# Kernel tuning notes

Measured on AMD Instinct MI355X. Metric: run time of the kernel, lower is better.

The kernel has to match this reference:

```python
import jax, jax.numpy as jnp
import numpy as np

BLOCK_SIZE = 32
HEADS = 8
DIM_HEAD = 64
ROPE_THETA = 10000.0


def rmsnorm(x, w):
    eps = jnp.finfo(x.dtype).eps
    var = jnp.mean(jnp.square(x), axis=-1, keepdims=True)
    return x * jax.lax.rsqrt(var + eps) * w


def rope_cos_sin(seq_len, dim_head):
    # lucidrains rotary-embedding-torch default: interleaved pairs, theta=10000
    inv_freq = 1.0 / (ROPE_THETA ** (jnp.arange(0, dim_head, 2, dtype=jnp.float32) / dim_head))
    freqs = jnp.arange(seq_len, dtype=jnp.float32)[:, None] * inv_freq[None, :]  # [S, Dh/2]
    return jnp.cos(freqs), jnp.sin(freqs)


def apply_rope(t, cos, sin):
    # t: [B, H, S, Dh], cos/sin: [S, Dh/2]
    t1 = t[..., 0::2]
    t2 = t[..., 1::2]
    out = jnp.stack([t1 * cos - t2 * sin, t1 * sin + t2 * cos], axis=-1)
    return out.reshape(t.shape)


def split_heads(x, h):
    b, n, _ = x.shape
    return x.reshape(b, n, h, -1).transpose(0, 2, 1, 3)  # b h n d


def forward(tokens, attn_norm_w, qkv_w, out_w, mix_w, mix_b,
            ff_norm_w, ff_in_w, ff_in_b, ff_out_w, ff_out_b, final_norm_w):
    B, S, D = tokens.shape
    L = qkv_w.shape[0]
    H, Dh = HEADS, DIM_HEAD
    scale = Dh ** -0.5
    cos, sin = rope_cos_sin(S, Dh)

    # block-causal mask: q_idx // block >= kv_idx // block
    idx = jnp.arange(S)
    allowed = (idx[:, None] // BLOCK_SIZE) >= (idx[None, :] // BLOCK_SIZE)  # [S, S] bool
    neg = -jnp.finfo(tokens.dtype).max

    t = tokens
    first_v = None
    for l in range(L):
        # --- block causal attention ---
        x = rmsnorm(t, attn_norm_w[l])
        qkv = x @ qkv_w[l]  # [B, S, 3*H*Dh]
        q, k, v = jnp.split(qkv, 3, axis=-1)
        q, k, v = split_heads(q, H), split_heads(k, H), split_heads(v, H)  # b h s d
        orig_v = v
        if l > 0:
            mix = jax.nn.sigmoid(x @ mix_w[l] + mix_b[l])  # [B, S, H]
            mix = mix.transpose(0, 2, 1)[..., None]  # [B, H, S, 1]
            v = v + mix * (first_v - v)  # lerp
        q = apply_rope(q, cos, sin)
        k = apply_rope(k, cos, sin)
        sim = jnp.einsum('bhid,bhjd->bhij', q * scale, k)
        sim = jnp.where(allowed, sim, neg)
        attn = jax.nn.softmax(sim, axis=-1)
        o = jnp.einsum('bhij,bhjd->bhid', attn, v)
        o = o.transpose(0, 2, 1, 3).reshape(B, S, H * Dh)
        t = t + o @ out_w[l]
        if first_v is None:
            first_v = orig_v
        # --- SwiGLU feedforward ---
        y = rmsnorm(t, ff_norm_w[l])
        h = y @ ff_in_w[l] + ff_in_b[l]
        a, g = jnp.split(h, 2, axis=-1)
        y = (a * jax.nn.gelu(g, approximate=False)) @ ff_out_w[l] + ff_out_b[l]
        t = t + y

    return rmsnorm(t, final_norm_w)


def setup_inputs():
    key = jax.random.key(0)
    B, S, D, L = 2, 2048, 512, 4
    Di = HEADS * DIM_HEAD  # 512
    Dhid = int(D * 4.0 * 2 / 3)  # 1365
    ks = jax.random.split(key, 8)
    s = 0.02
    return {
        'tokens': jax.random.normal(ks[0], (B, S, D), jnp.float32),
        'attn_norm_w': jnp.ones((L, D), jnp.float32),
        'qkv_w': jax.random.normal(ks[1], (L, D, 3 * Di), jnp.float32) * s,
        'out_w': jax.random.normal(ks[2], (L, Di, D), jnp.float32) * s,
        'mix_w': jax.random.normal(ks[3], (L, D, HEADS), jnp.float32) * s,
        'mix_b': jnp.zeros((L, HEADS), jnp.float32),
        'ff_norm_w': jnp.ones((L, D), jnp.float32),
        'ff_in_w': jax.random.normal(ks[4], (L, D, 2 * Dhid), jnp.float32) * s,
        'ff_in_b': jnp.zeros((L, 2 * Dhid), jnp.float32),
        'ff_out_w': jax.random.normal(ks[5], (L, Dhid, D), jnp.float32) * s,
        'ff_out_b': jnp.zeros((L, D), jnp.float32),
        'final_norm_w': jnp.ones((D,), jnp.float32),
    }


def reference(tokens, attn_norm_w, qkv_w, out_w, mix_w, mix_b,
              ff_norm_w, ff_in_w, ff_in_b, ff_out_w, ff_out_b, final_norm_w):
    return forward(tokens, attn_norm_w, qkv_w, out_w, mix_w, mix_b,
                   ff_norm_w, ff_in_w, ff_in_b, ff_out_w, ff_out_b, final_norm_w)
```

## Files before the change

### kernel.cpp

```cpp
#include <hip/hip_runtime.h>
#include <hip/hip_bf16.h>
#include <math.h>

typedef __bf16 bf16;
typedef bf16 bf16x8 __attribute__((ext_vector_type(8)));
typedef float f32x4 __attribute__((ext_vector_type(4)));

#define LDS16(gp, lp) __builtin_amdgcn_global_load_lds( \
    (const __attribute__((address_space(1))) unsigned int*)(gp), \
    (__attribute__((address_space(3))) unsigned int*)(lp), 16, 0, 0)

__device__ __forceinline__ int cumoff(int qt) {
  if (qt < 8)  return qt;
  if (qt < 16) return 8 + 2 * (qt - 8);
  if (qt < 24) return 24 + 3 * (qt - 16);
  return 48 + 4 * (qt - 24);
}

__global__ void convert_w_kernel(const float* __restrict__ W, bf16* __restrict__ WT,
                                 int K, int N, int Kp, int Np,
                                 size_t wstride, size_t wtstride)
{
  __shared__ float tile[32][33];
  const float* Wl = W + blockIdx.z * wstride;
  bf16* WTl = WT + blockIdx.z * wtstride;
  int k0 = blockIdx.x * 32, n0 = blockIdx.y * 32;
  int tx = threadIdx.x, ty = threadIdx.y;
  for (int i = ty; i < 32; i += 8) {
    int k = k0 + i, n = n0 + tx;
    tile[i][tx] = (k < K && n < N) ? Wl[(size_t)k * N + n] : 0.f;
  }
  __syncthreads();
  for (int i = ty; i < 32; i += 8) {
    int n = n0 + i, k = k0 + tx;
    if (n < Np && k < Kp) WTl[(size_t)n * Kp + k] = (bf16)tile[tx][i];
  }
}

__global__ __launch_bounds__(256)
void rope_kernel(float* __restrict__ tab)
{
  int idx = blockIdx.x * 256 + threadIdx.x;
  int s = idx >> 5, j = idx & 31;
  float invf = (float)exp((double)(2 * j) * -0.14391156847064293);
  float ang = (float)s * invf;
  float sn, cs;
  sincosf(ang, &sn, &cs);
  tab[idx] = cs;
  tab[65536 + idx] = sn;
}

template<bool BF16OUT>
__global__ __launch_bounds__(64)
void rmsnorm_kernel(const float* __restrict__ in, const float* __restrict__ wgt,
                    void* __restrict__ outp)
{
  int row = blockIdx.x, lane = threadIdx.x;
  const float* p = in + (size_t)row * 512;
  float4 v0 = *(const float4*)(p + lane * 4);
  float4 v1 = *(const float4*)(p + 256 + lane * 4);
  float ss = v0.x*v0.x + v0.y*v0.y + v0.z*v0.z + v0.w*v0.w
           + v1.x*v1.x + v1.y*v1.y + v1.z*v1.z + v1.w*v1.w;
  #pragma unroll
  for (int d = 1; d < 64; d <<= 1) ss += __shfl_xor(ss, d);
  float sc = rsqrtf(ss * (1.f / 512.f) + 1.1920929e-7f);
  float a0[4] = {v0.x, v0.y, v0.z, v0.w};
  float a1[4] = {v1.x, v1.y, v1.z, v1.w};
  #pragma unroll
  for (int i = 0; i < 4; ++i) {
    int c0 = lane * 4 + i, c1 = 256 + lane * 4 + i;
    float r0 = a0[i] * sc * wgt[c0];
    float r1 = a1[i] * sc * wgt[c1];
    if (BF16OUT) {
      ((bf16*)outp)[(size_t)row * 512 + c0] = (bf16)r0;
      ((bf16*)outp)[(size_t)row * 512 + c1] = (bf16)r1;
    } else {
      ((float*)outp)[(size_t)row * 512 + c0] = r0;
      ((float*)outp)[(size_t)row * 512 + c1] = r1;
    }
  }
}

__global__ __launch_bounds__(256)
void qkvpost_kernel(const float* __restrict__ qkv, const float* __restrict__ mb,
                    const float* __restrict__ rope, float* __restrict__ firstv,
                    bf16* __restrict__ qb, bf16* __restrict__ kb,
                    bf16* __restrict__ vT, int layer)
{
  int idx = blockIdx.x * 256 + threadIdx.x;
  int j = idx & 31;
  int s = (idx >> 5) & 2047;
  int bh = idx >> 16;
  int b = bh >> 3, h = bh & 7;
  size_t row = (size_t)b * 2048 + s;
  const float* base = qkv + row * 1664 + h * 64 + 2 * j;
  float q1 = base[0],    q2 = base[1];
  float k1 = base[512],  k2 = base[513];
  float v1 = base[1024], v2 = base[1025];
  float cs = rope[s * 32 + j];
  float sn = rope[65536 + s * 32 + j];
  size_t qoff = ((size_t)bh * 2048 + s) * 64 + 2 * j;
  qb[qoff]     = (bf16)((q1 * cs - q2 * sn) * 0.125f);
  qb[qoff + 1] = (bf16)((q1 * sn + q2 * cs) * 0.125f);
  kb[qoff]     = (bf16)(k1 * cs - k2 * sn);
  kb[qoff + 1] = (bf16)(k1 * sn + k2 * cs);
  if (layer == 0) {
    firstv[qoff] = v1; firstv[qoff + 1] = v2;
  } else {
    float logit = qkv[row * 1664 + 1536 + h] + mb[h];
    float mx = 1.f / (1.f + __expf(-logit));
    v1 += mx * (firstv[qoff] - v1);
    v2 += mx * (firstv[qoff + 1] - v2);
  }
  vT[((size_t)bh * 64 + 2 * j) * 2048 + s]     = (bf16)v1;
  vT[((size_t)bh * 64 + 2 * j + 1) * 2048 + s] = (bf16)v2;
}

__global__ __launch_bounds__(256, 3)
void attn_kernel(const bf16* __restrict__ Q, const bf16* __restrict__ Kmat,
                 const bf16* __restrict__ VT, float* __restrict__ Opart,
                 float* __restrict__ mlbuf)
{
  __shared__ __align__(16) bf16 smK[2][8 * 512];
  __shared__ __align__(16) bf16 smV[2][8 * 512];
  __shared__ __align__(16) bf16 smP[4][16 * 72];
  const int bid = blockIdx.x;
  const int bh = bid / 80;
  const int r80 = bid - bh * 80;
  int qt, chunk;
  if (r80 < 8)       { qt = r80; chunk = 0; }
  else if (r80 < 24) { qt = 8 + ((r80 - 8) >> 1);  chunk = (r80 - 8) & 1; }
  else if (r80 < 48) { int t = r80 - 24; qt = 16 + t / 3; chunk = t - (qt - 16) * 3; }
  else               { int t = r80 - 48; qt = 24 + (t >> 2); chunk = t & 3; }
  const int jt0 = chunk * 8;
  const int njt = min(jt0 + 8, qt + 1) - jt0;

  const int tid = threadIdx.x;
  const int w = tid >> 6, lane = tid & 63;
  const int c = lane & 15, quad = lane >> 4;

  const size_t qrow0 = (size_t)bh * 2048 + qt * 64 + w * 16;
  bf16x8 aQ0 = *(const bf16x8*)(Q + (qrow0 + c) * 64 + quad * 8);
  bf16x8 aQ1 = *(const bf16x8*)(Q + (qrow0 + c) * 64 + 32 + quad * 8);

  const bf16* Kg = Kmat + ((size_t)bh * 2048 + w * 16 + c) * 64 + quad * 8;
  const bf16* Vg = VT + ((size_t)bh * 64 + w * 16 + c) * 2048 + quad * 8;

  {
    const bf16* kp = Kg + (size_t)jt0 * 4096;
    const bf16* vp = Vg + jt0 * 64;
    LDS16(kp,      smK[0] + w * 1024);
    LDS16(kp + 32, smK[0] + w * 1024 + 512);
    LDS16(vp,      smV[0] + w * 1024);
    LDS16(vp + 32, smV[0] + w * 1024 + 512);
  }

  f32x4 o[4] = {{0,0,0,0},{0,0,0,0},{0,0,0,0},{0,0,0,0}};
  float mrow[4] = {-3.0e38f, -3.0e38f, -3.0e38f, -3.0e38f};
  float lrow[4] = {0.f, 0.f, 0.f, 0.f};

  for (int j = 0; j < njt; ++j) {
    const int b = j & 1;
    const int jt = jt0 + j;
    __syncthreads();
    if (j + 1 < njt) {
      const bf16* kp = Kg + (size_t)(jt + 1) * 4096;
      const bf16* vp = Vg + (jt + 1) * 64;
      bf16* kd = smK[1 - b] + w * 1024;
      bf16* vd = smV[1 - b] + w * 1024;
      LDS16(kp,      kd);
      LDS16(kp + 32, kd + 512);
      LDS16(vp,      vd);
      LDS16(vp + 32, vd + 512);
    }

    f32x4 s[4];
    #pragma unroll
    for (int nt = 0; nt < 4; ++nt) {
      bf16x8 bK0 = *(const bf16x8*)(smK[b] + (nt * 2) * 512 + lane * 8);
      bf16x8 bK1 = *(const bf16x8*)(smK[b] + (nt * 2 + 1) * 512 + lane * 8);
      f32x4 acc = {0.f, 0.f, 0.f, 0.f};
      acc = __builtin_amdgcn_mfma_f32_16x16x32_bf16(aQ0, bK0, acc, 0, 0, 0);
      acc = __builtin_amdgcn_mfma_f32_16x16x32_bf16(aQ1, bK1, acc, 0, 0, 0);
      s[nt] = acc;
    }
    if (jt == qt && w < 2) {
      #pragma unroll
      for (int r = 0; r < 4; ++r) { s[2][r] = -3.0e38f; s[3][r] = -3.0e38f; }
    }

    #pragma unroll
    for (int r = 0; r < 4; ++r) {
      float smax = fmaxf(fmaxf(s[0][r], s[1][r]), fmaxf(s[2][r], s[3][r]));
      #pragma unroll
      for (int d = 1; d < 16; d <<= 1) smax = fmaxf(smax, __shfl_xor(smax, d));
      float mnew = fmaxf(mrow[r], smax);
      float alpha = __expf(mrow[r] - mnew);
      mrow[r] = mnew;
      float p0 = __expf(s[0][r] - mnew);
      float p1 = __expf(s[1][r] - mnew);
      float p2 = __expf(s[2][r] - mnew);
      float p3 = __expf(s[3][r] - mnew);
      float rsum = (p0 + p1) + (p2 + p3);
      #pragma unroll
      for (int d = 1; d < 16; d <<= 1) rsum += __shfl_xor(rsum, d);
      lrow[r] = lrow[r] * alpha + rsum;
      o[0][r] *= alpha; o[1][r] *= alpha; o[2][r] *= alpha; o[3][r] *= alpha;
      bf16* pp = smP[w] + (quad * 4 + r) * 72 + c;
      pp[0]  = (bf16)p0;
      pp[16] = (bf16)p1;
      pp[32] = (bf16)p2;
      pp[48] = (bf16)p3;
    }
    asm volatile("s_waitcnt lgkmcnt(0)" ::: "memory");

    #pragma unroll
    for (int ks2 = 0; ks2 < 2; ++ks2) {
      bf16x8 aP = *(const bf16x8*)(smP[w] + c * 72 + ks2 * 32 + quad * 8);
      #pragma unroll
      for (int nt = 0; nt < 4; ++nt) {
        bf16x8 bV = *(const bf16x8*)(smV[b] + (nt * 2 + ks2) * 512 + lane * 8);
        o[nt] = __builtin_amdgcn_mfma_f32_16x16x32_bf16(aP, bV, o[nt], 0, 0, 0);
      }
    }
  }

  const int slot = bh * 80 + cumoff(qt) + chunk;
  float* Op = Opart + (size_t)slot * 4096;
  #pragma unroll
  for (int r = 0; r < 4; ++r) {
    int row = w * 16 + quad * 4 + r;
    #pragma unroll
    for (int nt = 0; nt < 4; ++nt)
      Op[row * 64 + nt * 16 + c] = o[nt][r];
    if (c == 0) {
      mlbuf[slot * 128 + row] = mrow[r];
      mlbuf[slot * 128 + 64 + row] = lrow[r];
    }
  }
}

__global__ __launch_bounds__(256)
void attn_combine_kernel(const float* __restrict__ Opart, const float* __restrict__ mlbuf,
                         bf16* __restrict__ Omat)
{
  const int qt = blockIdx.x, bh = blockIdx.y;
  const int nch = (qt >> 3) + 1;
  const int base = bh * 80 + cumoff(qt);
  const int tid = threadIdx.x;
  const int row = tid >> 2, cg = tid & 3;

  float mv[4], lv[4];
  float M = -3.0e38f;
  #pragma unroll
  for (int ch = 0; ch < 4; ++ch) {
    if (ch < nch) {
      mv[ch] = mlbuf[(base + ch) * 128 + row];
      lv[ch] = mlbuf[(base + ch) * 128 + 64 + row];
      M = fmaxf(M, mv[ch]);
    } else { mv[ch] = -3.0e38f; lv[ch] = 0.f; }
  }
  float L = 0.f, wgt[4];
  #pragma unroll
  for (int ch = 0; ch < 4; ++ch) {
    wgt[ch] = __expf(mv[ch] - M);
    L += lv[ch] * wgt[ch];
  }
  float inv = 1.f / L;

  f32x4 acc[4] = {{0,0,0,0},{0,0,0,0},{0,0,0,0},{0,0,0,0}};
  #pragma unroll
  for (int ch = 0; ch < 4; ++ch) {
    if (ch < nch) {
      const f32x4* p = (const f32x4*)(Opart + (size_t)(base + ch) * 4096 + row * 64 + cg * 16);
      #pragma unroll
      for (int i = 0; i < 4; ++i) acc[i] += wgt[ch] * p[i];
    }
  }
  const int b = bh >> 3, h = bh & 7;
  bf16* op = Omat + ((size_t)b * 2048 + qt * 64 + row) * 512 + h * 64 + cg * 16;
  #pragma unroll
  for (int i = 0; i < 4; ++i)
    #pragma unroll
    for (int j = 0; j < 4; ++j)
      op[i * 4 + j] = (bf16)(acc[i][j] * inv);
}

template<int MODE>
__global__ __launch_bounds__(256, 2)
void gemm_kernel(const bf16* __restrict__ A, const bf16* __restrict__ WT,
                 const float* __restrict__ bias, int n_bias,
                 const float* __restrict__ Tin, void* __restrict__ outp,
                 int K, int N)
{
  __shared__ __align__(16) bf16 smA[8 * 512];
  __shared__ __align__(16) bf16 smB[8 * 512];
  const int tid = threadIdx.x;
  const int w = tid >> 6, lane = tid & 63;
  const int c = lane & 15, quad = lane >> 4;
  const int wy = w >> 1, wx = w & 1;
  const int bm = blockIdx.y * 128, bn = blockIdx.x * 128;

  f32x4 acc[4][4] = {};

  const bf16* Ag0 = A  + (size_t)(bm + (w * 2)     * 16 + c) * K + quad * 8;
  const bf16* Ag1 = A  + (size_t)(bm + (w * 2 + 1) * 16 + c) * K + quad * 8;
  const bf16* Bg0 = WT + (size_t)(bn + (w * 2)     * 16 + c) * K + quad * 8;
  const bf16* Bg1 = WT + (size_t)(bn + (w * 2 + 1) * 16 + c) * K + quad * 8;
  bf16* la0 = smA + (w * 2) * 512;
  bf16* la1 = smA + (w * 2 + 1) * 512;
  bf16* lb0 = smB + (w * 2) * 512;
  bf16* lb1 = smB + (w * 2 + 1) * 512;

  const int NK = K >> 5;
  for (int kk = 0; kk < NK; ++kk) {
    const int ko = kk * 32;
    LDS16(Ag0 + ko, la0);
    LDS16(Ag1 + ko, la1);
    LDS16(Bg0 + ko, lb0);
    LDS16(Bg1 + ko, lb1);
    __syncthreads();
    bf16x8 af[4], bfr[4];
    #pragma unroll
    for (int mt = 0; mt < 4; ++mt)
      af[mt] = *(const bf16x8*)(smA + (wy * 4 + mt) * 512 + lane * 8);
    #pragma unroll
    for (int nt = 0; nt < 4; ++nt)
      bfr[nt] = *(const bf16x8*)(smB + (wx * 4 + nt) * 512 + lane * 8);
    #pragma unroll
    for (int mt = 0; mt < 4; ++mt)
      #pragma unroll
      for (int nt = 0; nt < 4; ++nt)
        acc[mt][nt] = __builtin_amdgcn_mfma_f32_16x16x32_bf16(af[mt], bfr[nt], acc[mt][nt], 0, 0, 0);
    __syncthreads();
  }

  const int r0 = bm + wy * 64;
  const int c0 = bn + wx * 64;
  #pragma unroll
  for (int mt = 0; mt < 4; ++mt) {
    #pragma unroll
    for (int nt = 0; nt < 4; ++nt) {
      #pragma unroll
      for (int r = 0; r < 4; ++r) {
        size_t row = (size_t)(r0 + mt * 16 + quad * 4 + r);
        int col = c0 + nt * 16 + c;
        float v = acc[mt][nt][r];
        float bv = (bias != nullptr && col < n_bias) ? bias[col] : 0.f;
        if (MODE == 2) {
          ((float*)outp)[row * N + col] = Tin[row * N + col] + v + bv;
        } else if (MODE == 1) {
          ((float*)outp)[row * N + col] = v;
        } else {
          ((bf16*)outp)[row * N + col] = (bf16)(v + bv);
        }
      }
    }
  }
}

template<int MODE>
__global__ __launch_bounds__(256, 4)
void gemm64_kernel(const bf16* __restrict__ A, const bf16* __restrict__ WT,
                   const float* __restrict__ bias, int n_bias,
                   const float* __restrict__ Tin, void* __restrict__ outp,
                   int K, int N)
{
  __shared__ __align__(16) bf16 smA[4 * 512];
  __shared__ __align__(16) bf16 smB[4 * 512];
  const int tid = threadIdx.x;
  const int w = tid >> 6, lane = tid & 63;
  const int c = lane & 15, quad = lane >> 4;
  const int wy = w >> 1, wx = w & 1;
  const int bm = blockIdx.y * 64, bn = blockIdx.x * 64;

  f32x4 acc[2][2] = {};

  const bf16* Ag = A  + (size_t)(bm + w * 16 + c) * K + quad * 8;
  const bf16* Bg = WT + (size_t)(bn + w * 16 + c) * K + quad * 8;
  bf16* la = smA + w * 512;
  bf16* lb = smB + w * 512;

  const int NK = K >> 5;
  for (int kk = 0; kk < NK; ++kk) {
    const int ko = kk * 32;
    LDS16(Ag + ko, la);
    LDS16(Bg + ko, lb);
    __syncthreads();
    bf16x8 af[2], bfr[2];
    #pragma unroll
    for (int mt = 0; mt < 2; ++mt)
      af[mt] = *(const bf16x8*)(smA + (wy * 2 + mt) * 512 + lane * 8);
    #pragma unroll
    for (int nt = 0; nt < 2; ++nt)
      bfr[nt] = *(const bf16x8*)(smB + (wx * 2 + nt) * 512 + lane * 8);
    #pragma unroll
    for (int mt = 0; mt < 2; ++mt)
      #pragma unroll
      for (int nt = 0; nt < 2; ++nt)
        acc[mt][nt] = __builtin_amdgcn_mfma_f32_16x16x32_bf16(af[mt], bfr[nt], acc[mt][nt], 0, 0, 0);
    __syncthreads();
  }

  const int r0 = bm + wy * 32;
  const int c0 = bn + wx * 32;
  #pragma unroll
  for (int mt = 0; mt < 2; ++mt) {
    #pragma unroll
    for (int nt = 0; nt < 2; ++nt) {
      #pragma unroll
      for (int r = 0; r < 4; ++r) {
        size_t row = (size_t)(r0 + mt * 16 + quad * 4 + r);
        int col = c0 + nt * 16 + c;
        float v = acc[mt][nt][r];
        float bv = (bias != nullptr && col < n_bias) ? bias[col] : 0.f;
        if (MODE == 2) {
          ((float*)outp)[row * N + col] = Tin[row * N + col] + v + bv;
        } else if (MODE == 1) {
          ((float*)outp)[row * N + col] = v;
        } else {
          ((bf16*)outp)[row * N + col] = (bf16)(v + bv);
        }
      }
    }
  }
}

__global__ __launch_bounds__(256)
void act_kernel(const bf16* __restrict__ h, bf16* __restrict__ act)
{
  int col = blockIdx.x * 256 + threadIdx.x;
  int row = blockIdx.y;
  if (col >= 1376) return;
  float v = 0.f;
  if (col < 1365) {
    float a = (float)h[(size_t)row * 2816 + col];
    float g = (float)h[(size_t)row * 2816 + 1365 + col];
    v = a * 0.5f * g * (1.f + erff(g * 0.70710678118654752f));
  }
  act[(size_t)row * 1376 + col] = (bf16)v;
}

extern "C" void kernel_launch(void* const* d_in, const int* in_sizes, int n_in,
                              void* d_out, int out_size, void* d_ws, size_t ws_size,
                              hipStream_t stream)
{
  const float* tokens  = (const float*)d_in[0];
  const float* anw     = (const float*)d_in[1];
  const float* qkvw    = (const float*)d_in[2];
  const float* outw    = (const float*)d_in[3];
  const float* mixw    = (const float*)d_in[4];
  const float* mixbias = (const float*)d_in[5];
  const float* fnw     = (const float*)d_in[6];
  const float* ffiw    = (const float*)d_in[7];
  const float* ffib    = (const float*)d_in[8];
  const float* ffow    = (const float*)d_in[9];
  const float* ffob    = (const float*)d_in[10];
  const float* finw    = (const float*)d_in[11];
  float* outp = (float*)d_out;

  char* ws = (char*)d_ws;
  size_t off = 0;
  auto alloc = [&](size_t bytes) -> char* {
    char* p = ws + off;
    off += (bytes + 255) & ~(size_t)255;
    return p;
  };
  bf16* wtq    = (bf16*)alloc((size_t)4 * 1664 * 512 * 2);
  bf16* wto    = (bf16*)alloc((size_t)4 * 512 * 512 * 2);
  bf16* wtfi   = (bf16*)alloc((size_t)4 * 2816 * 512 * 2);
  bf16* wtfo   = (bf16*)alloc((size_t)4 * 512 * 1376 * 2);
  float* tbuf  = (float*)alloc((size_t)4096 * 512 * 4);
  bf16* xb     = (bf16*)alloc((size_t)4096 * 512 * 2);
  bf16* yb     = (bf16*)alloc((size_t)4096 * 512 * 2);
  float* qkvb  = (float*)alloc((size_t)4096 * 1664 * 4);
  float* fv    = (float*)alloc((size_t)16 * 2048 * 64 * 4);
  bf16* qb     = (bf16*)alloc((size_t)16 * 2048 * 64 * 2);
  bf16* kbuf   = (bf16*)alloc((size_t)16 * 2048 * 64 * 2);
  bf16* vT     = (bf16*)alloc((size_t)16 * 2048 * 64 * 2);
  bf16* ob     = (bf16*)alloc((size_t)4096 * 512 * 2);
  bf16* hb     = (bf16*)alloc((size_t)4096 * 2816 * 2);
  bf16* actb   = (bf16*)alloc((size_t)4096 * 1376 * 2);
  float* rope  = (float*)alloc((size_t)2 * 65536 * 4);
  float* mlbuf = (float*)alloc((size_t)1280 * 128 * 4);
  float* Opart = qkvb;

  dim3 tcv(32, 8);
  convert_w_kernel<<<dim3(16, 48, 4), tcv, 0, stream>>>(
      qkvw, wtq, 512, 1536, 512, 1536, (size_t)512 * 1536, (size_t)1664 * 512);
  convert_w_kernel<<<dim3(16, 4, 4), tcv, 0, stream>>>(
      mixw, wtq + (size_t)1536 * 512, 512, 8, 512, 128, (size_t)512 * 8, (size_t)1664 * 512);
  convert_w_kernel<<<dim3(16, 16, 4), tcv, 0, stream>>>(
      outw, wto, 512, 512, 512, 512, (size_t)512 * 512, (size_t)512 * 512);
  convert_w_kernel<<<dim3(16, 88, 4), tcv, 0, stream>>>(
      ffiw, wtfi, 512, 2730, 512, 2816, (size_t)512 * 2730, (size_t)2816 * 512);
  convert_w_kernel<<<dim3(43, 16, 4), tcv, 0, stream>>>(
      ffow, wtfo, 1365, 512, 1376, 512, (size_t)1365 * 512, (size_t)1376 * 512);
  rope_kernel<<<256, 256, 0, stream>>>(rope);
  hipMemcpyAsync(tbuf, tokens, (size_t)4096 * 512 * 4, hipMemcpyDeviceToDevice, stream);

  for (int l = 0; l < 4; ++l) {
    rmsnorm_kernel<true><<<4096, 64, 0, stream>>>(tbuf, anw + l * 512, xb);
    gemm_kernel<1><<<dim3(13, 32), 256, 0, stream>>>(
        xb, wtq + (size_t)l * 1664 * 512, nullptr, 0, nullptr, qkvb, 512, 1664);
    qkvpost_kernel<<<4096, 256, 0, stream>>>(qkvb, mixbias + l * 8, rope, fv, qb, kbuf, vT, l);
    attn_kernel<<<1280, 256, 0, stream>>>(qb, kbuf, vT, Opart, mlbuf);
    attn_combine_kernel<<<dim3(32, 16), 256, 0, stream>>>(Opart, mlbuf, ob);
    gemm64_kernel<2><<<dim3(8, 64), 256, 0, stream>>>(
        ob, wto + (size_t)l * 512 * 512, nullptr, 0, tbuf, tbuf, 512, 512);
    rmsnorm_kernel<true><<<4096, 64, 0, stream>>>(tbuf, fnw + l * 512, yb);
    gemm_kernel<0><<<dim3(22, 32), 256, 0, stream>>>(
        yb, wtfi + (size_t)l * 2816 * 512, ffib + (size_t)l * 2730, 2730, nullptr, hb, 512, 2816);
    act_kernel<<<dim3(6, 4096), 256, 0, stream>>>(hb, actb);
    gemm64_kernel<2><<<dim3(8, 64), 256, 0, stream>>>(
        actb, wtfo + (size_t)l * 512 * 1376, ffob + (size_t)l * 512, 512, tbuf, tbuf, 1376, 512);
  }
  rmsnorm_kernel<false><<<4096, 64, 0, stream>>>(tbuf, finw, outp);
}
```

Measured before the change: 874.2 us.

## Process 128 query rows per attention block and emit QKV projection in bf16

The attention kernel now handles a 128-row query tile per block: each wave owns 32 rows as two 16-row MFMA sub-tiles, so every K/V tile staged in LDS is reused by twice as many queries and the grid shrinks from 1280 to 640 blocks. Waves skip key tiles that lie wholly beyond their causal limit, and the partial-output and combine indexing are reworked for the larger tile. Separately, the QKV GEMM writes bf16 instead of fp32 (mode 0 instead of mode 1), halving that intermediate's traffic into qkvpost but rounding q/k/v and the mix logit to bf16 before RoPE and the lerp. The larger tile raises register and LDS use per block and leaves waves idle on the diagonal tiles.

Result: no change. 873.3 us (-0.1%).

```diff
diff --git a/kernel.cpp b/kernel.cpp
--- a/kernel.cpp
+++ b/kernel.cpp
@@ -10,11 +10,11 @@
     (const __attribute__((address_space(1))) unsigned int*)(gp), \
     (__attribute__((address_space(3))) unsigned int*)(lp), 16, 0, 0)
 
-__device__ __forceinline__ int cumoff(int qt) {
-  if (qt < 8)  return qt;
-  if (qt < 16) return 8 + 2 * (qt - 8);
-  if (qt < 24) return 24 + 3 * (qt - 16);
-  return 48 + 4 * (qt - 24);
+__device__ __forceinline__ int cumoff2(int qtp) {
+  if (qtp < 4)  return qtp;
+  if (qtp < 8)  return 4 + 2 * (qtp - 4);
+  if (qtp < 12) return 12 + 3 * (qtp - 8);
+  return 24 + 4 * (qtp - 12);
 }
 
 __global__ void convert_w_kernel(const float* __restrict__ W, bf16* __restrict__ WT,
@@ -82,7 +82,7 @@
 }
 
 __global__ __launch_bounds__(256)
-void qkvpost_kernel(const float* __restrict__ qkv, const float* __restrict__ mb,
+void qkvpost_kernel(const bf16* __restrict__ qkv, const float* __restrict__ mb,
                     const float* __restrict__ rope, float* __restrict__ firstv,
                     bf16* __restrict__ qb, bf16* __restrict__ kb,
                     bf16* __restrict__ vT, int layer)
@@ -93,10 +93,10 @@
   int bh = idx >> 16;
   int b = bh >> 3, h = bh & 7;
   size_t row = (size_t)b * 2048 + s;
-  const float* base = qkv + row * 1664 + h * 64 + 2 * j;
-  float q1 = base[0],    q2 = base[1];
-  float k1 = base[512],  k2 = base[513];
-  float v1 = base[1024], v2 = base[1025];
+  const bf16* base = qkv + row * 1664 + h * 64 + 2 * j;
+  float q1 = (float)base[0],    q2 = (float)base[1];
+  float k1 = (float)base[512],  k2 = (float)base[513];
+  float v1 = (float)base[1024], v2 = (float)base[1025];
   float cs = rope[s * 32 + j];
   float sn = rope[65536 + s * 32 + j];
   size_t qoff = ((size_t)bh * 2048 + s) * 64 + 2 * j;
@@ -107,7 +107,7 @@
   if (layer == 0) {
     firstv[qoff] = v1; firstv[qoff + 1] = v2;
   } else {
-    float logit = qkv[row * 1664 + 1536 + h] + mb[h];
+    float logit = (float)qkv[row * 1664 + 1536 + h] + mb[h];
     float mx = 1.f / (1.f + __expf(-logit));
     v1 += mx * (firstv[qoff] - v1);
     v2 += mx * (firstv[qoff + 1] - v2);
@@ -123,25 +123,30 @@
 {
   __shared__ __align__(16) bf16 smK[2][8 * 512];
   __shared__ __align__(16) bf16 smV[2][8 * 512];
-  __shared__ __align__(16) bf16 smP[4][16 * 72];
+  __shared__ __align__(16) bf16 smP[4][2][16 * 72];
   const int bid = blockIdx.x;
-  const int bh = bid / 80;
-  const int r80 = bid - bh * 80;
-  int qt, chunk;
-  if (r80 < 8)       { qt = r80; chunk = 0; }
-  else if (r80 < 24) { qt = 8 + ((r80 - 8) >> 1);  chunk = (r80 - 8) & 1; }
-  else if (r80 < 48) { int t = r80 - 24; qt = 16 + t / 3; chunk = t - (qt - 16) * 3; }
-  else               { int t = r80 - 48; qt = 24 + (t >> 2); chunk = t & 3; }
+  const int bh = bid / 40;
+  const int r40 = bid - bh * 40;
+  int qtp, chunk;
+  if (r40 < 4)       { qtp = r40; chunk = 0; }
+  else if (r40 < 12) { qtp = 4 + ((r40 - 4) >> 1);  chunk = (r40 - 4) & 1; }
+  else if (r40 < 24) { int t = r40 - 12; qtp = 8 + t / 3; chunk = t - (qtp - 8) * 3; }
+  else               { int t = r40 - 24; qtp = 12 + (t >> 2); chunk = t & 3; }
   const int jt0 = chunk * 8;
-  const int njt = min(jt0 + 8, qt + 1) - jt0;
+  const int njt = min(jt0 + 8, 2 * qtp + 2) - jt0;
 
   const int tid = threadIdx.x;
   const int w = tid >> 6, lane = tid & 63;
   const int c = lane & 15, quad = lane >> 4;
-
-  const size_t qrow0 = (size_t)bh * 2048 + qt * 64 + w * 16;
-  bf16x8 aQ0 = *(const bf16x8*)(Q + (qrow0 + c) * 64 + quad * 8);
-  bf16x8 aQ1 = *(const bf16x8*)(Q + (qrow0 + c) * 64 + 32 + quad * 8);
+  const int jtmax_w = (qtp * 4 + w) >> 1;
+
+  const size_t qrow0 = (size_t)bh * 2048 + qtp * 128 + w * 32;
+  bf16x8 aQ[2][2];
+  #pragma unroll
+  for (int m = 0; m < 2; ++m) {
+    aQ[m][0] = *(const bf16x8*)(Q + (qrow0 + m * 16 + c) * 64 + quad * 8);
+    aQ[m][1] = *(const bf16x8*)(Q + (qrow0 + m * 16 + c) * 64 + 32 + quad * 8);
+  }
 
   const bf16* Kg = Kmat + ((size_t)bh * 2048 + w * 16 + c) * 64 + quad * 8;
   const bf16* Vg = VT + ((size_t)bh * 64 + w * 16 + c) * 2048 + quad * 8;
@@ -155,9 +160,12 @@
     LDS16(vp + 32, smV[0] + w * 1024 + 512);
   }
 
-  f32x4 o[4] = {{0,0,0,0},{0,0,0,0},{0,0,0,0},{0,0,0,0}};
-  float mrow[4] = {-3.0e38f, -3.0e38f, -3.0e38f, -3.0e38f};
-  float lrow[4] = {0.f, 0.f, 0.f, 0.f};
+  f32x4 o[2][4] = {};
+  float mrow[2][4], lrow[2][4];
+  #pragma unroll
+  for (int m = 0; m < 2; ++m)
+    #pragma unroll
+    for (int r = 0; r < 4; ++r) { mrow[m][r] = -3.0e38f; lrow[m][r] = 0.f; }
 
   for (int j = 0; j < njt; ++j) {
     const int b = j & 1;
@@ -173,69 +181,84 @@
       LDS16(vp,      vd);
       LDS16(vp + 32, vd + 512);
     }
-
-    f32x4 s[4];
+    if (jt > jtmax_w) continue;
+
+    f32x4 s[2][4];
     #pragma unroll
     for (int nt = 0; nt < 4; ++nt) {
       bf16x8 bK0 = *(const bf16x8*)(smK[b] + (nt * 2) * 512 + lane * 8);
       bf16x8 bK1 = *(const bf16x8*)(smK[b] + (nt * 2 + 1) * 512 + lane * 8);
-      f32x4 acc = {0.f, 0.f, 0.f, 0.f};
-      acc = __builtin_amdgcn_mfma_f32_16x16x32_bf16(aQ0, bK0, acc, 0, 0, 0);
-      acc = __builtin_amdgcn_mfma_f32_16x16x32_bf16(aQ1, bK1, acc, 0, 0, 0);
-      s[nt] = acc;
-    }
-    if (jt == qt && w < 2) {
-      #pragma unroll
-      for (int r = 0; r < 4; ++r) { s[2][r] = -3.0e38f; s[3][r] = -3.0e38f; }
-    }
-
+      #pragma unroll
+      for (int m = 0; m < 2; ++m) {
+        f32x4 acc = {0.f, 0.f, 0.f, 0.f};
+        acc = __builtin_amdgcn_mfma_f32_16x16x32_bf16(aQ[m][0], bK0, acc, 0, 0, 0);
+        acc = __builtin_amdgcn_mfma_f32_16x16x32_bf16(aQ[m][1], bK1, acc, 0, 0, 0);
+        s[m][nt] = acc;
+      }
+    }
+    if (2 * jt + 1 > 4 * qtp + w) {
+      #pragma unroll
+      for (int m = 0; m < 2; ++m)
+        #pragma unroll
+        for (int r = 0; r < 4; ++r) { s[m][2][r] = -3.0e38f; s[m][3][r] = -3.0e38f; }
+    }
+
+    #pragma unroll
+    for (int m = 0; m < 2; ++m) {
+      #pragma unroll
+      for (int r = 0; r < 4; ++r) {
+        float smax = fmaxf(fmaxf(s[m][0][r], s[m][1][r]), fmaxf(s[m][2][r], s[m][3][r]));
+        #pragma unroll
+        for (int d = 1; d < 16; d <<= 1) smax = fmaxf(smax, __shfl_xor(smax, d));
+        float mnew = fmaxf(mrow[m][r], smax);
+        float alpha = __expf(mrow[m][r] - mnew);
+        mrow[m][r] = mnew;
+        float p0 = __expf(s[m][0][r] - mnew);
+        float p1 = __expf(s[m][1][r] - mnew);
+        float p2 = __expf(s[m][2][r] - mnew);
+        float p3 = __expf(s[m][3][r] - mnew);
+        float rsum = (p0 + p1) + (p2 + p3);
+        #pragma unroll
+        for (int d = 1; d < 16; d <<= 1) rsum += __shfl_xor(rsum, d);
+        lrow[m][r] = lrow[m][r] * alpha + rsum;
+        o[m][0][r] *= alpha; o[m][1][r] *= alpha; o[m][2][r] *= alpha; o[m][3][r] *= alpha;
+        bf16* pp = smP[w][m] + (quad * 4 + r) * 72 + c;
+        pp[0]  = (bf16)p0;
+        pp[16] = (bf16)p1;
+        pp[32] = (bf16)p2;
+        pp[48] = (bf16)p3;
+      }
+    }
+    asm volatile("s_waitcnt lgkmcnt(0)" ::: "memory");
+
+    #pragma unroll
+    for (int ks2 = 0; ks2 < 2; ++ks2) {
+      #pragma unroll
+      for (int m = 0; m < 2; ++m) {
+        bf16x8 aP = *(const bf16x8*)(smP[w][m] + c * 72 + ks2 * 32 + quad * 8);
+        #pragma unroll
+        for (int nt = 0; nt < 4; ++nt) {
+          bf16x8 bV = *(const bf16x8*)(smV[b] + (nt * 2 + ks2) * 512 + lane * 8);
+          o[m][nt] = __builtin_amdgcn_mfma_f32_16x16x32_bf16(aP, bV, o[m][nt], 0, 0, 0);
+        }
+      }
+    }
+  }
+
+  const int slot = bh * 40 + cumoff2(qtp) + chunk;
+  float* Op = Opart + (size_t)slot * 8192;
+  #pragma unroll
+  for (int m = 0; m < 2; ++m) {
     #pragma unroll
     for (int r = 0; r < 4; ++r) {
-      float smax = fmaxf(fmaxf(s[0][r], s[1][r]), fmaxf(s[2][r], s[3][r]));
-      #pragma unroll
-      for (int d = 1; d < 16; d <<= 1) smax = fmaxf(smax, __shfl_xor(smax, d));
-      float mnew = fmaxf(mrow[r], smax);
-      float alpha = __expf(mrow[r] - mnew);
-      mrow[r] = mnew;
-      float p0 = __expf(s[0][r] - mnew);
-      float p1 = __expf(s[1][r] - mnew);
-      float p2 = __expf(s[2][r] - mnew);
-      float p3 = __expf(s[3][r] - mnew);
-      float rsum = (p0 + p1) + (p2 + p3);
-      #pragma unroll
-      for (int d = 1; d < 16; d <<= 1) rsum += __shfl_xor(rsum, d);
-      lrow[r] = lrow[r] * alpha + rsum;
-      o[0][r] *= alpha; o[1][r] *= alpha; o[2][r] *= alpha; o[3][r] *= alpha;
-      bf16* pp = smP[w] + (quad * 4 + r) * 72 + c;
-      pp[0]  = (bf16)p0;
-      pp[16] = (bf16)p1;
-      pp[32] = (bf16)p2;
-      pp[48] = (bf16)p3;
-    }
-    asm volatile("s_waitcnt lgkmcnt(0)" ::: "memory");
-
-    #pragma unroll
-    for (int ks2 = 0; ks2 < 2; ++ks2) {
-      bf16x8 aP = *(const bf16x8*)(smP[w] + c * 72 + ks2 * 32 + quad * 8);
-      #pragma unroll
-      for (int nt = 0; nt < 4; ++nt) {
-        bf16x8 bV = *(const bf16x8*)(smV[b] + (nt * 2 + ks2) * 512 + lane * 8);
-        o[nt] = __builtin_amdgcn_mfma_f32_16x16x32_bf16(aP, bV, o[nt], 0, 0, 0);
+      int prow = w * 32 + m * 16 + quad * 4 + r;
+      #pragma unroll
+      for (int nt = 0; nt < 4; ++nt)
+        Op[prow * 64 + nt * 16 + c] = o[m][nt][r];
+      if (c == 0) {
+        mlbuf[slot * 256 + prow] = mrow[m][r];
+        mlbuf[slot * 256 + 128 + prow] = lrow[m][r];
       }
-    }
-  }
-
-  const int slot = bh * 80 + cumoff(qt) + chunk;
-  float* Op = Opart + (size_t)slot * 4096;
-  #pragma unroll
-  for (int r = 0; r < 4; ++r) {
-    int row = w * 16 + quad * 4 + r;
-    #pragma unroll
-    for (int nt = 0; nt < 4; ++nt)
-      Op[row * 64 + nt * 16 + c] = o[nt][r];
-    if (c == 0) {
-      mlbuf[slot * 128 + row] = mrow[r];
-      mlbuf[slot * 128 + 64 + row] = lrow[r];
     }
   }
 }
@@ -245,18 +268,20 @@
                          bf16* __restrict__ Omat)
 {
   const int qt = blockIdx.x, bh = blockIdx.y;
-  const int nch = (qt >> 3) + 1;
-  const int base = bh * 80 + cumoff(qt);
+  const int qtp = qt >> 1;
+  const int nch = (2 * qtp + 9) >> 3;
+  const int base = bh * 40 + cumoff2(qtp);
   const int tid = threadIdx.x;
   const int row = tid >> 2, cg = tid & 3;
+  const int prow = (qt & 1) * 64 + row;
 
   float mv[4], lv[4];
   float M = -3.0e38f;
   #pragma unroll
   for (int ch = 0; ch < 4; ++ch) {
     if (ch < nch) {
-      mv[ch] = mlbuf[(base + ch) * 128 + row];
-      lv[ch] = mlbuf[(base + ch) * 128 + 64 + row];
+      mv[ch] = mlbuf[(base + ch) * 256 + prow];
+      lv[ch] = mlbuf[(base + ch) * 256 + 128 + prow];
       M = fmaxf(M, mv[ch]);
     } else { mv[ch] = -3.0e38f; lv[ch] = 0.f; }
   }
@@ -272,7 +297,7 @@
   #pragma unroll
   for (int ch = 0; ch < 4; ++ch) {
     if (ch < nch) {
-      const f32x4* p = (const f32x4*)(Opart + (size_t)(base + ch) * 4096 + row * 64 + cg * 16);
+      const f32x4* p = (const f32x4*)(Opart + (size_t)(base + ch) * 8192 + prow * 64 + cg * 16);
       #pragma unroll
       for (int i = 0; i < 4; ++i) acc[i] += wgt[ch] * p[i];
     }
@@ -473,7 +498,7 @@
   float* tbuf  = (float*)alloc((size_t)4096 * 512 * 4);
   bf16* xb     = (bf16*)alloc((size_t)4096 * 512 * 2);
   bf16* yb     = (bf16*)alloc((size_t)4096 * 512 * 2);
-  float* qkvb  = (float*)alloc((size_t)4096 * 1664 * 4);
+  char* qkvraw = alloc((size_t)4096 * 1664 * 4);
   float* fv    = (float*)alloc((size_t)16 * 2048 * 64 * 4);
   bf16* qb     = (bf16*)alloc((size_t)16 * 2048 * 64 * 2);
   bf16* kbuf   = (bf16*)alloc((size_t)16 * 2048 * 64 * 2);
@@ -482,8 +507,9 @@
   bf16* hb     = (bf16*)alloc((size_t)4096 * 2816 * 2);
   bf16* actb   = (bf16*)alloc((size_t)4096 * 1376 * 2);
   float* rope  = (float*)alloc((size_t)2 * 65536 * 4);
-  float* mlbuf = (float*)alloc((size_t)1280 * 128 * 4);
-  float* Opart = qkvb;
+  float* mlbuf = (float*)alloc((size_t)640 * 256 * 4);
+  bf16* qkvbf  = (bf16*)qkvraw;
+  float* Opart = (float*)qkvraw;
 
   dim3 tcv(32, 8);
   convert_w_kernel<<<dim3(16, 48, 4), tcv, 0, stream>>>(
@@ -501,10 +527,10 @@
 
   for (int l = 0; l < 4; ++l) {
     rmsnorm_kernel<true><<<4096, 64, 0, stream>>>(tbuf, anw + l * 512, xb);
-    gemm_kernel<1><<<dim3(13, 32), 256, 0, stream>>>(
-        xb, wtq + (size_t)l * 1664 * 512, nullptr, 0, nullptr, qkvb, 512, 1664);
-    qkvpost_kernel<<<4096, 256, 0, stream>>>(qkvb, mixbias + l * 8, rope, fv, qb, kbuf, vT, l);
-    attn_kernel<<<1280, 256, 0, stream>>>(qb, kbuf, vT, Opart, mlbuf);
+    gemm_kernel<0><<<dim3(13, 32), 256, 0, stream>>>(
+        xb, wtq + (size_t)l * 1664 * 512, nullptr, 0, nullptr, qkvbf, 512, 1664);
+    qkvpost_kernel<<<4096, 256, 0, stream>>>(qkvbf, mixbias + l * 8, rope, fv, qb, kbuf, vT, l);
+    attn_kernel<<<640, 256, 0, stream>>>(qb, kbuf, vT, Opart, mlbuf);
     attn_combine_kernel<<<dim3(32, 16), 256, 0, stream>>>(Opart, mlbuf, ob);
     gemm64_kernel<2><<<dim3(8, 64), 256, 0, stream>>>(
         ob, wto + (size_t)l * 512 * 512, nullptr, 0, tbuf, tbuf, 512, 512);
```
